# Kernel tuning notes

Hardware: AMD Instinct MI355X
Metric: run time of the kernel (lower is better)

The kernel has to match this reference:

```python
import jax, jax.numpy as jnp
import numpy as np

N_NODES = 32000
N_EDGES = 320000
N_GRAPHS = 1600
HID = 128
RBF = 32
ZDIM = 2 * HID + RBF  # CGConv concat dim = 288


def setup_inputs() -> dict:
    key = jax.random.key(0)
    ks = jax.random.split(key, 20)
    inp = {
        "x": jax.random.randint(ks[0], (N_NODES,), 0, 100),
        "edge_index": jax.random.randint(ks[1], (2, N_EDGES), 0, N_NODES),
        "edge_attr": jax.random.normal(ks[2], (N_EDGES, RBF), dtype=jnp.float32),
        "batch": jnp.sort(jax.random.randint(ks[3], (N_NODES,), 0, N_GRAPHS)),
        "emb": jax.random.normal(ks[4], (100, HID), dtype=jnp.float32) * 0.02,
    }
    s = 1.0 / np.sqrt(ZDIM)
    for i, k0 in zip((1, 2, 3), range(5, 11, 2)):
        inp[f"Wf{i}"] = jax.random.uniform(ks[k0], (ZDIM, HID), jnp.float32, -s, s)
        inp[f"bf{i}"] = jnp.zeros((HID,), jnp.float32)
        inp[f"Ws{i}"] = jax.random.uniform(ks[k0 + 1], (ZDIM, HID), jnp.float32, -s, s)
        inp[f"bs{i}"] = jnp.zeros((HID,), jnp.float32)
    sl = 1.0 / np.sqrt(HID)
    inp["Wlin"] = jax.random.uniform(ks[11], (HID, HID), jnp.float32, -sl, sl)
    inp["blin"] = jnp.zeros((HID,), jnp.float32)
    return inp


def _cgconv(h, src, dst, ea, Wf, bf, Ws, bs):
    # PyG CGConv: z = [x_i, x_j, e_ij]; msg = sigmoid(lin_f(z)) * softplus(lin_s(z)); out = x + sum_j msg
    z = jnp.concatenate([h[dst], h[src], ea], axis=1)  # [E, 288]
    msg = jax.nn.sigmoid(z @ Wf + bf) * jax.nn.softplus(z @ Ws + bs)  # [E, 128]
    return h + jax.ops.segment_sum(msg, dst, num_segments=N_NODES)


def reference(x, edge_index, edge_attr, batch, emb,
              Wf1, bf1, Ws1, bs1, Wf2, bf2, Ws2, bs2, Wf3, bf3, Ws3, bs3,
              Wlin, blin):
    src, dst = edge_index[0], edge_index[1]
    h = emb[x]  # [N, 128] embedding lookup
    h = jax.nn.relu(_cgconv(h, src, dst, edge_attr, Wf1, bf1, Ws1, bs1))
    h = jax.nn.relu(_cgconv(h, src, dst, edge_attr, Wf2, bf2, Ws2, bs2))
    h = jax.nn.relu(_cgconv(h, src, dst, edge_attr, Wf3, bf3, Ws3, bs3))
    # global mean pool over graphs
    sums = jax.ops.segment_sum(h, batch, num_segments=N_GRAPHS)  # [G, 128]
    cnt = jax.ops.segment_sum(jnp.ones((N_NODES,), h.dtype), batch, num_segments=N_GRAPHS)
    pooled = sums / jnp.maximum(cnt, 1.0)[:, None]
    return pooled @ Wlin + blin  # [G, 128]
```

## Files before the change

kernel.cpp:

```cpp
#include <hip/hip_runtime.h>
#include <math.h>

#define NN 32000
#define NE 320000
#define NG 1600
#define LOG2E 1.4426950408889634f
#define LN2   0.6931471805599453f

using frag_ab = __attribute__((ext_vector_type(8))) short;
using frag_cd = __attribute__((ext_vector_type(4))) float;
typedef float v2f __attribute__((ext_vector_type(2)));

static __device__ __forceinline__ unsigned short f2bf(float f) {
  unsigned u = __builtin_bit_cast(unsigned, f);
  unsigned r = u + 0x7fff + ((u >> 16) & 1);
  return (unsigned short)(r >> 16);
}
static __device__ __forceinline__ float bflo(unsigned u) {
  return __builtin_bit_cast(float, u << 16);
}
static __device__ __forceinline__ float bfhi(unsigned u) {
  return __builtin_bit_cast(float, u & 0xffff0000u);
}
static __device__ __forceinline__ float bfs(unsigned short u) {
  return __builtin_bit_cast(float, (unsigned)u << 16);
}
static __device__ __forceinline__ v2f unpk(unsigned u) {
  return (v2f){bflo(u), bfhi(u)};
}

__global__ __launch_bounds__(256) void k_misc(const int* __restrict__ x,
                                              const float* __restrict__ emb,
                                              const float* __restrict__ Wf1, const float* __restrict__ Ws1,
                                              const float* __restrict__ Wf2, const float* __restrict__ Ws2,
                                              const float* __restrict__ Wf3, const float* __restrict__ Ws3,
                                              unsigned short* __restrict__ hb,
                                              unsigned short* __restrict__ accumb,
                                              unsigned short* __restrict__ wedge,
                                              unsigned short* __restrict__ wgemm) {
  int b = blockIdx.x;
  int tid = threadIdx.x;
  if (b < 2000) {
    int idx = b * 256 + tid;
    int n = idx >> 4;
    int c8 = (idx & 15) << 3;
    const float* e = emb + (size_t)x[n] * 128 + c8;
    float4 v0 = *(const float4*)e;
    float4 v1 = *(const float4*)(e + 4);
    ushort4 p0, p1;
    p0.x = f2bf(v0.x); p0.y = f2bf(v0.y); p0.z = f2bf(v0.z); p0.w = f2bf(v0.w);
    p1.x = f2bf(v1.x); p1.y = f2bf(v1.y); p1.z = f2bf(v1.z); p1.w = f2bf(v1.w);
    unsigned short* hbp = hb + (size_t)n * 128 + c8;
    *(ushort4*)hbp = p0;
    *(ushort4*)(hbp + 4) = p1;
    *(uint4*)(accumb + (size_t)n * 128 + c8) = make_uint4(0, 0, 0, 0);
  } else if (b < 2096) {
    int idx = (b - 2000) * 256 + tid;
    int l = idx >> 13;
    int r = idx & 8191;
    int j = r & 7;
    int lane = (r >> 3) & 63;
    int wt = r >> 9;
    int w = wt >> 2, t = wt & 3;
    int c = lane & 15, q = lane >> 4;
    int k = q * 8 + j;
    const float* Wf = (l == 0) ? Wf1 : (l == 1) ? Wf2 : Wf3;
    const float* Ws = (l == 0) ? Ws1 : (l == 1) ? Ws2 : Ws3;
    const float* W = (t < 2) ? Wf : Ws;
    int ch = w * 32 + 2 * c + (t & 1);
    wedge[(size_t)l * 8192 + r] = f2bf(W[(size_t)(256 + k) * 128 + ch] * LOG2E);
  } else {
    int idx = (b - 2096) * 256 + tid;
    int l = idx >> 16;
    int r = idx & 65535;
    int cc = r >> 7;
    int k = r & 127;
    int p = (cc & ~31) + ((cc & 15) << 1) + ((cc >> 4) & 1);
    int ph = p & 255;
    int j = ph >> 2, sub = ph & 3;
    const float* Wf = (l == 0) ? Wf1 : (l == 1) ? Wf2 : Wf3;
    const float* Ws = (l == 0) ? Ws1 : (l == 1) ? Ws2 : Ws3;
    const float* W = (sub < 2) ? Wf : Ws;
    int ch = 2 * j + (sub & 1);
    int krow = ((p < 256) ? 0 : 128) + k;
    wgemm[(size_t)l * 65536 + cc * 128 + k] = f2bf(W[(size_t)krow * 128 + ch] * LOG2E);
  }
}

__global__ __launch_bounds__(256) void k_histb(const int* __restrict__ ei,
                                               const int* __restrict__ batch,
                                               int* __restrict__ counts,
                                               int* __restrict__ starts) {
  int b = blockIdx.x;
  int tid = threadIdx.x;
  if (b < 1250) {
    int e = b * 256 + tid;
    atomicAdd(counts + ei[NE + e], 1);
  } else {
    int n = (b - 1250) * 256 + tid;
    if (n > NN) return;
    if (n == NN) {
      starts[NG] = NN;
      int last = batch[NN - 1];
      for (int g = last + 1; g < NG; ++g) starts[g] = NN;
    } else if (n == 0) {
      int bb = batch[0];
      for (int g = 0; g <= bb; ++g) starts[g] = 0;
    } else {
      int b0 = batch[n - 1], b1 = batch[n];
      for (int g = b0 + 1; g <= b1; ++g) starts[g] = n;
    }
  }
}

__global__ __launch_bounds__(1024) void k_scan(const int* __restrict__ counts,
                                               int* __restrict__ offs) {
  __shared__ int part[1024];
  __shared__ int carry_s;
  int t = threadIdx.x;
  if (t == 0) carry_s = 0;
  __syncthreads();
  for (int chunk = 0; chunk < 4; ++chunk) {
    int base = chunk * 8192 + t * 8;
    int4 a = make_int4(0, 0, 0, 0), bq = make_int4(0, 0, 0, 0);
    bool full = (base + 8 <= NN);
    if (full) {
      a = *(const int4*)(counts + base);
      bq = *(const int4*)(counts + base + 4);
    }
    int e1 = a.x, e2 = e1 + a.y, e3 = e2 + a.z, e4 = e3 + a.w;
    int e5 = e4 + bq.x, e6 = e5 + bq.y, e7 = e6 + bq.z;
    int run = e7 + bq.w;
    part[t] = run;
    __syncthreads();
    for (int off = 1; off < 1024; off <<= 1) {
      int v = (t >= off) ? part[t - off] : 0;
      __syncthreads();
      part[t] += v;
      __syncthreads();
    }
    int excl = carry_s + ((t == 0) ? 0 : part[t - 1]);
    if (full) {
      int4 o0 = make_int4(excl, excl + e1, excl + e2, excl + e3);
      int4 o1 = make_int4(excl + e4, excl + e5, excl + e6, excl + e7);
      *(int4*)(offs + base) = o0;
      *(int4*)(offs + base + 4) = o1;
    }
    __syncthreads();
    if (t == 0) carry_s += part[1023];
    __syncthreads();
  }
}

__global__ __launch_bounds__(256) void k_scat1(const int* __restrict__ ei,
                                               int* __restrict__ offs,
                                               int* __restrict__ perm) {
  int e = blockIdx.x * 256 + threadIdx.x;
  int d = ei[NE + e];
  int pos = atomicAdd(offs + d, 1);
  perm[pos] = e;
}

__global__ __launch_bounds__(256) void k_s2g(const unsigned short* __restrict__ hb,
                                             const unsigned short* __restrict__ wgemmL,
                                             unsigned short* __restrict__ T,
                                             const int* __restrict__ ei,
                                             const float* __restrict__ ea,
                                             const int* __restrict__ perm,
                                             int* __restrict__ srcp,
                                             int* __restrict__ dstp,
                                             unsigned short* __restrict__ eab) {
  __shared__ short sA[64 * 136];
  __shared__ short sB[128 * 136];
  __shared__ int se[64];
  int b = blockIdx.x;
  int tid = threadIdx.x;
  if (b < 2000) {
    int m0 = (b >> 2) * 64;
    int n0 = (b & 3) * 128;
#pragma unroll
    for (int i = 0; i < 4; ++i) {
      int idx = tid + i * 256;
      int row = idx >> 4, chk = idx & 15;
      uint4 v = *(const uint4*)(hb + (size_t)(m0 + row) * 128 + chk * 8);
      *(uint4*)&sA[row * 136 + chk * 8] = v;
    }
#pragma unroll
    for (int i = 0; i < 8; ++i) {
      int idx = tid + i * 256;
      int col = idx >> 4, chk = idx & 15;
      uint4 v = *(const uint4*)(wgemmL + (size_t)(n0 + col) * 128 + chk * 8);
      *(uint4*)&sB[col * 136 + chk * 8] = v;
    }
    __syncthreads();
    int w = tid >> 6, lane = tid & 63, c = lane & 15, q = lane >> 4;
    frag_cd acc[4][2];
#pragma unroll
    for (int mt = 0; mt < 4; ++mt)
#pragma unroll
      for (int t = 0; t < 2; ++t) acc[mt][t] = (frag_cd){0.f, 0.f, 0.f, 0.f};
#pragma unroll
    for (int ks = 0; ks < 4; ++ks) {
      frag_ab Af[4], Bf[2];
#pragma unroll
      for (int mt = 0; mt < 4; ++mt)
        Af[mt] = *(const frag_ab*)&sA[(mt * 16 + c) * 136 + ks * 32 + q * 8];
#pragma unroll
      for (int t = 0; t < 2; ++t)
        Bf[t] = *(const frag_ab*)&sB[(w * 32 + t * 16 + c) * 136 + ks * 32 + q * 8];
#pragma unroll
      for (int mt = 0; mt < 4; ++mt)
#pragma unroll
        for (int t = 0; t < 2; ++t)
          acc[mt][t] = __builtin_amdgcn_mfma_f32_16x16x32_bf16(Af[mt], Bf[t], acc[mt][t], 0, 0, 0);
    }
    int nbase = n0 + w * 32 + 2 * c;
#pragma unroll
    for (int mt = 0; mt < 4; ++mt) {
#pragma unroll
      for (int r = 0; r < 4; ++r) {
        int node = m0 + mt * 16 + q * 4 + r;
        unsigned pk = (unsigned)f2bf(acc[mt][0][r]) | ((unsigned)f2bf(acc[mt][1][r]) << 16);
        *(unsigned*)(T + (size_t)node * 512 + nbase) = pk;
      }
    }
  } else {
    int base = (b - 2000) * 64;
    if (tid < 64) {
      int e = perm[base + tid];
      se[tid] = e;
      srcp[base + tid] = ei[e];
      dstp[base + tid] = ei[NE + e];
    }
    __syncthreads();
    int x = tid >> 2;
    int ck = tid & 3;
    int e = se[x];
    const float* a = ea + (size_t)e * 32 + ck * 8;
    float4 v0 = *(const float4*)a;
    float4 v1 = *(const float4*)(a + 4);
    int p = (((x >> 2) & 3) << 4) | ((x >> 4) << 2) | (x & 3);
    unsigned short* q = eab + (size_t)(base + p) * 32 + ck * 8;
    ushort4 o0, o1;
    o0.x = f2bf(v0.x); o0.y = f2bf(v0.y); o0.z = f2bf(v0.z); o0.w = f2bf(v0.w);
    o1.x = f2bf(v1.x); o1.y = f2bf(v1.y); o1.z = f2bf(v1.z); o1.w = f2bf(v1.w);
    *(ushort4*)q = o0;
    *(ushort4*)(q + 4) = o1;
  }
}

__global__ __launch_bounds__(256) void k_ugemm(unsigned short* __restrict__ hb,
                                               unsigned short* __restrict__ accumb,
                                               const unsigned short* __restrict__ wgemmL,
                                               unsigned short* __restrict__ T) {
  __shared__ short sA[64 * 136];
  __shared__ short sB[128 * 136];
  int m0 = blockIdx.x * 64;
  int tid = threadIdx.x;
#pragma unroll
  for (int i = 0; i < 4; ++i) {
    int idx = tid + i * 256;
    int row = idx >> 4, chk = idx & 15;
    size_t off = (size_t)(m0 + row) * 128 + chk * 8;
    uint4 a = *(uint4*)(accumb + off);
    uint4 hv = *(uint4*)(hb + off);
    float r0 = fmaxf(bflo(hv.x) + bflo(a.x), 0.f);
    float r1 = fmaxf(bfhi(hv.x) + bfhi(a.x), 0.f);
    float r2 = fmaxf(bflo(hv.y) + bflo(a.y), 0.f);
    float r3 = fmaxf(bfhi(hv.y) + bfhi(a.y), 0.f);
    float r4 = fmaxf(bflo(hv.z) + bflo(a.z), 0.f);
    float r5 = fmaxf(bfhi(hv.z) + bfhi(a.z), 0.f);
    float r6 = fmaxf(bflo(hv.w) + bflo(a.w), 0.f);
    float r7 = fmaxf(bfhi(hv.w) + bfhi(a.w), 0.f);
    uint4 o;
    o.x = (unsigned)f2bf(r0) | ((unsigned)f2bf(r1) << 16);
    o.y = (unsigned)f2bf(r2) | ((unsigned)f2bf(r3) << 16);
    o.z = (unsigned)f2bf(r4) | ((unsigned)f2bf(r5) << 16);
    o.w = (unsigned)f2bf(r6) | ((unsigned)f2bf(r7) << 16);
    *(uint4*)(hb + off) = o;
    *(uint4*)(accumb + off) = make_uint4(0, 0, 0, 0);
    *(uint4*)&sA[row * 136 + chk * 8] = o;
  }
  int w = tid >> 6, lane = tid & 63, c = lane & 15, q = lane >> 4;
#pragma unroll 1
  for (int nb = 0; nb < 4; ++nb) {
    int n0 = nb * 128;
    __syncthreads();
#pragma unroll
    for (int i = 0; i < 8; ++i) {
      int idx = tid + i * 256;
      int col = idx >> 4, chk = idx & 15;
      uint4 v = *(const uint4*)(wgemmL + (size_t)(n0 + col) * 128 + chk * 8);
      *(uint4*)&sB[col * 136 + chk * 8] = v;
    }
    __syncthreads();
    frag_cd acc[4][2];
#pragma unroll
    for (int mt = 0; mt < 4; ++mt)
#pragma unroll
      for (int t = 0; t < 2; ++t) acc[mt][t] = (frag_cd){0.f, 0.f, 0.f, 0.f};
#pragma unroll
    for (int ks = 0; ks < 4; ++ks) {
      frag_ab Af[4], Bf[2];
#pragma unroll
      for (int mt = 0; mt < 4; ++mt)
        Af[mt] = *(const frag_ab*)&sA[(mt * 16 + c) * 136 + ks * 32 + q * 8];
#pragma unroll
      for (int t = 0; t < 2; ++t)
        Bf[t] = *(const frag_ab*)&sB[(w * 32 + t * 16 + c) * 136 + ks * 32 + q * 8];
#pragma unroll
      for (int mt = 0; mt < 4; ++mt)
#pragma unroll
        for (int t = 0; t < 2; ++t)
          acc[mt][t] = __builtin_amdgcn_mfma_f32_16x16x32_bf16(Af[mt], Bf[t], acc[mt][t], 0, 0, 0);
    }
    int nbase = n0 + w * 32 + 2 * c;
#pragma unroll
    for (int mt = 0; mt < 4; ++mt) {
#pragma unroll
      for (int r = 0; r < 4; ++r) {
        int node = m0 + mt * 16 + q * 4 + r;
        unsigned pk = (unsigned)f2bf(acc[mt][0][r]) | ((unsigned)f2bf(acc[mt][1][r]) << 16);
        *(unsigned*)(T + (size_t)node * 512 + nbase) = pk;
      }
    }
  }
}

__global__ __launch_bounds__(512) void k_edge(const int* __restrict__ srcp,
                                              const int* __restrict__ dstp,
                                              const unsigned short* __restrict__ eab,
                                              const unsigned short* __restrict__ T,
                                              const unsigned short* __restrict__ wedgeL,
                                              const float* __restrict__ bf,
                                              const float* __restrict__ bs,
                                              unsigned short* __restrict__ accumb) {
  __shared__ short sA[128 * 40];
  __shared__ short sB[8192];
  __shared__ float sbf[128], sbs[128];
  __shared__ int sSrc[128], sDst[128];
  int tid = threadIdx.x;
  int e0 = blockIdx.x * 128;
  {
    int row = tid >> 2, qq = tid & 3;
    uint4 v = *(const uint4*)(eab + (size_t)e0 * 32 + tid * 8);
    *(uint4*)&sA[row * 40 + qq * 8] = v;
  }
#pragma unroll
  for (int i = 0; i < 2; ++i) {
    int idx = tid + i * 512;
    uint4 v = *(const uint4*)(wedgeL + idx * 8);
    *(uint4*)&sB[idx * 8] = v;
  }
  if (tid < 128) {
    sbf[tid] = bf[tid] * LOG2E;
    sbs[tid] = bs[tid] * LOG2E;
  } else if (tid < 256) {
    sSrc[tid - 128] = srcp[e0 + tid - 128] * 512 + 256;
  } else if (tid < 384) {
    sDst[tid - 256] = dstp[e0 + tid - 256] * 512;
  }
  __syncthreads();

  int wave = tid >> 6;
  int w = wave & 3;
  int eh = (wave >> 2) * 64;
  int lane = tid & 63;
  int c = lane & 15;
  int q = lane >> 4;

  int ch = w * 32 + 2 * c;
  int jo = ch * 2;
  v2f bfv = {sbf[ch], sbf[ch + 1]};
  v2f bsv = {sbs[ch], sbs[ch + 1]};

  frag_ab Af[4], Bf[4];
#pragma unroll
  for (int et = 0; et < 4; ++et)
    Af[et] = *(const frag_ab*)&sA[(eh + et * 16 + c) * 40 + q * 8];
#pragma unroll
  for (int t = 0; t < 4; ++t)
    Bf[t] = *(const frag_ab*)&sB[((w * 4 + t) * 64 + lane) * 8];

  frag_cd acc[4][4];
#pragma unroll
  for (int et = 0; et < 4; ++et) {
    acc[et][0] = (frag_cd){bfv.x, bfv.x, bfv.x, bfv.x};
    acc[et][1] = (frag_cd){bfv.y, bfv.y, bfv.y, bfv.y};
    acc[et][2] = (frag_cd){bsv.x, bsv.x, bsv.x, bsv.x};
    acc[et][3] = (frag_cd){bsv.y, bsv.y, bsv.y, bsv.y};
  }
#pragma unroll
  for (int et = 0; et < 4; ++et)
#pragma unroll
    for (int t = 0; t < 4; ++t)
      acc[et][t] = __builtin_amdgcn_mfma_f32_16x16x32_bf16(Af[et], Bf[t], acc[et][t], 0, 0, 0);

  int le0 = eh + q * 16;
  int prevd = sDst[le0];
  v2f av = {0.f, 0.f};

  uint2 dvb[2][4], svb[2][4];
#pragma unroll
  for (int i = 0; i < 4; ++i) {
    int e = le0 + i;
    dvb[0][i] = *(const uint2*)(T + sDst[e] + jo);
    svb[0][i] = *(const uint2*)(T + sSrc[e] + jo);
  }
#pragma unroll
  for (int g = 0; g < 4; ++g) {
    int cur = g & 1, nxt = cur ^ 1;
    if (g < 3) {
#pragma unroll
      for (int i = 0; i < 4; ++i) {
        int e = le0 + (g + 1) * 4 + i;
        dvb[nxt][i] = *(const uint2*)(T + sDst[e] + jo);
        svb[nxt][i] = *(const uint2*)(T + sSrc[e] + jo);
      }
    }
    v2f m[4];
#pragma unroll
    for (int i = 0; i < 4; ++i) {
      v2f xf = (v2f){acc[g][0][i], acc[g][1][i]} + unpk(dvb[cur][i].x) + unpk(svb[cur][i].x);
      v2f xs = (v2f){acc[g][2][i], acc[g][3][i]} + unpk(dvb[cur][i].y) + unpk(svb[cur][i].y);
      float g0 = __builtin_amdgcn_rcpf(1.f + __builtin_amdgcn_exp2f(-xf.x));
      float g1 = __builtin_amdgcn_rcpf(1.f + __builtin_amdgcn_exp2f(-xf.y));
      float sp0 = fmaxf(xs.x, 0.f) + __builtin_amdgcn_logf(1.f + __builtin_amdgcn_exp2f(-fabsf(xs.x)));
      float sp1 = fmaxf(xs.y, 0.f) + __builtin_amdgcn_logf(1.f + __builtin_amdgcn_exp2f(-fabsf(xs.y)));
      m[i] = (v2f){g0 * sp0, g1 * sp1};
    }
#pragma unroll
    for (int i = 0; i < 4; ++i) {
      int d = sDst[le0 + g * 4 + i];
      if (d != prevd) {
        v2f o = av * LN2;
        unsigned pk = (unsigned)f2bf(o.x) | ((unsigned)f2bf(o.y) << 16);
        unsigned short* p = accumb + (size_t)(prevd >> 2) + ch;
        asm volatile("global_atomic_pk_add_bf16 %0, %1, off" :: "v"(p), "v"(pk) : "memory");
        av = (v2f){0.f, 0.f};
        prevd = d;
      }
      av += m[i];
    }
  }
  {
    v2f o = av * LN2;
    unsigned pk = (unsigned)f2bf(o.x) | ((unsigned)f2bf(o.y) << 16);
    unsigned short* p = accumb + (size_t)(prevd >> 2) + ch;
    asm volatile("global_atomic_pk_add_bf16 %0, %1, off" :: "v"(p), "v"(pk) : "memory");
  }
}

__global__ __launch_bounds__(128) void k_pool_final(const unsigned short* __restrict__ hb,
                                                    const unsigned short* __restrict__ accumb,
                                                    const int* __restrict__ starts,
                                                    const float* __restrict__ Wlin,
                                                    const float* __restrict__ blin,
                                                    float* __restrict__ out) {
  __shared__ float p[128];
  int g = blockIdx.x, c = threadIdx.x;
  int s0 = starts[g], s1 = starts[g + 1];
  float acc = 0.f;
  for (int n = s0; n < s1; ++n) {
    float hv = bfs(hb[(size_t)n * 128 + c]);
    float av = bfs(accumb[(size_t)n * 128 + c]);
    acc += fmaxf(hv + av, 0.f);
  }
  float inv = 1.f / fmaxf((float)(s1 - s0), 1.f);
  p[c] = acc * inv;
  __syncthreads();
  float o = blin[c];
#pragma unroll 8
  for (int k = 0; k < 128; ++k) o += p[k] * Wlin[k * 128 + c];
  out[(size_t)g * 128 + c] = o;
}

extern "C" void kernel_launch(void* const* d_in, const int* in_sizes, int n_in,
                              void* d_out, int out_size, void* d_ws, size_t ws_size,
                              hipStream_t stream) {
  const int* x = (const int*)d_in[0];
  const int* ei = (const int*)d_in[1];
  const float* ea = (const float*)d_in[2];
  const int* batch = (const int*)d_in[3];
  const float* emb = (const float*)d_in[4];
  const float* Wf[3] = {(const float*)d_in[5], (const float*)d_in[9], (const float*)d_in[13]};
  const float* bf[3] = {(const float*)d_in[6], (const float*)d_in[10], (const float*)d_in[14]};
  const float* Wsm[3] = {(const float*)d_in[7], (const float*)d_in[11], (const float*)d_in[15]};
  const float* bs[3] = {(const float*)d_in[8], (const float*)d_in[12], (const float*)d_in[16]};
  const float* Wlin = (const float*)d_in[17];
  const float* blin = (const float*)d_in[18];
  float* out = (float*)d_out;

  char* ws = (char*)d_ws;
  unsigned short* hb = (unsigned short*)ws;     ws += (size_t)NN * 128 * 2;
  unsigned short* accumb = (unsigned short*)ws; ws += (size_t)NN * 128 * 2;
  unsigned short* T = (unsigned short*)ws;      ws += (size_t)NN * 512 * 2;
  unsigned short* eab = (unsigned short*)ws;    ws += (size_t)NE * 32 * 2;
  unsigned short* wedge = (unsigned short*)ws;  ws += 3 * 8192 * 2;
  unsigned short* wgemm = (unsigned short*)ws;  ws += 3 * 65536 * 2;
  int* counts = (int*)ws;                       ws += (size_t)NN * 4;
  int* offs = (int*)ws;                         ws += (size_t)NN * 4;
  int* srcp = (int*)ws;                         ws += (size_t)NE * 4;
  int* dstp = (int*)ws;                         ws += (size_t)NE * 4;
  int* perm = (int*)ws;                         ws += (size_t)NE * 4;
  int* starts = (int*)ws;                       ws += (size_t)(NG + 1) * 4;

  hipMemsetAsync(counts, 0, (size_t)NN * 4, stream);
  k_misc<<<2864, 256, 0, stream>>>(x, emb, Wf[0], Wsm[0], Wf[1], Wsm[1], Wf[2], Wsm[2],
                                   hb, accumb, wedge, wgemm);
  k_histb<<<1376, 256, 0, stream>>>(ei, batch, counts, starts);
  k_scan<<<1, 1024, 0, stream>>>(counts, offs);
  k_scat1<<<1250, 256, 0, stream>>>(ei, offs, perm);
  k_s2g<<<7000, 256, 0, stream>>>(hb, wgemm, T, ei, ea, perm, srcp, dstp, eab);
  for (int l = 0; l < 3; ++l) {
    if (l > 0)
      k_ugemm<<<500, 256, 0, stream>>>(hb, accumb, wgemm + (size_t)l * 65536, T);
    k_edge<<<2500, 512, 0, stream>>>(srcp, dstp, eab, T, wedge + (size_t)l * 8192,
                                     bf[l], bs[l], accumb);
  }
  k_pool_final<<<1600, 128, 0, stream>>>(hb, accumb, starts, Wlin, blin, out);
}
```

Before: 346.3 us.

## Merge weight prep with histogram and fuse embedding lookup into first GEMM

Combines the weight-conversion kernel and the edge-histogram/graph-start kernel into one launch. The embedding lookup, bf16 conversion and accumulator zeroing move into the layer-1 node GEMM. Each GEMM block now builds its 64-row A tile directly from the embedding and loops over all four 128-column B tiles, instead of four blocks each reloading A from global memory. This removes one launch and a round trip of the node features through memory, at the cost of fewer, longer GEMM blocks (500 instead of 2000) with a serial loop over N tiles.

```diff
diff --git a/kernel.cpp b/kernel.cpp
--- a/kernel.cpp
+++ b/kernel.cpp
@@ -29,33 +29,19 @@
   return (v2f){bflo(u), bfhi(u)};
 }
 
-__global__ __launch_bounds__(256) void k_misc(const int* __restrict__ x,
-                                              const float* __restrict__ emb,
-                                              const float* __restrict__ Wf1, const float* __restrict__ Ws1,
-                                              const float* __restrict__ Wf2, const float* __restrict__ Ws2,
-                                              const float* __restrict__ Wf3, const float* __restrict__ Ws3,
-                                              unsigned short* __restrict__ hb,
-                                              unsigned short* __restrict__ accumb,
-                                              unsigned short* __restrict__ wedge,
-                                              unsigned short* __restrict__ wgemm) {
+__global__ __launch_bounds__(256) void k_prephist(const float* __restrict__ Wf1, const float* __restrict__ Ws1,
+                                                  const float* __restrict__ Wf2, const float* __restrict__ Ws2,
+                                                  const float* __restrict__ Wf3, const float* __restrict__ Ws3,
+                                                  const int* __restrict__ ei,
+                                                  const int* __restrict__ batch,
+                                                  unsigned short* __restrict__ wedge,
+                                                  unsigned short* __restrict__ wgemm,
+                                                  int* __restrict__ counts,
+                                                  int* __restrict__ starts) {
   int b = blockIdx.x;
   int tid = threadIdx.x;
-  if (b < 2000) {
+  if (b < 96) {
     int idx = b * 256 + tid;
-    int n = idx >> 4;
-    int c8 = (idx & 15) << 3;
-    const float* e = emb + (size_t)x[n] * 128 + c8;
-    float4 v0 = *(const float4*)e;
-    float4 v1 = *(const float4*)(e + 4);
-    ushort4 p0, p1;
-    p0.x = f2bf(v0.x); p0.y = f2bf(v0.y); p0.z = f2bf(v0.z); p0.w = f2bf(v0.w);
-    p1.x = f2bf(v1.x); p1.y = f2bf(v1.y); p1.z = f2bf(v1.z); p1.w = f2bf(v1.w);
-    unsigned short* hbp = hb + (size_t)n * 128 + c8;
-    *(ushort4*)hbp = p0;
-    *(ushort4*)(hbp + 4) = p1;
-    *(uint4*)(accumb + (size_t)n * 128 + c8) = make_uint4(0, 0, 0, 0);
-  } else if (b < 2096) {
-    int idx = (b - 2000) * 256 + tid;
     int l = idx >> 13;
     int r = idx & 8191;
     int j = r & 7;
@@ -69,8 +55,8 @@
     const float* W = (t < 2) ? Wf : Ws;
     int ch = w * 32 + 2 * c + (t & 1);
     wedge[(size_t)l * 8192 + r] = f2bf(W[(size_t)(256 + k) * 128 + ch] * LOG2E);
-  } else {
-    int idx = (b - 2096) * 256 + tid;
+  } else if (b < 864) {
+    int idx = (b - 96) * 256 + tid;
     int l = idx >> 16;
     int r = idx & 65535;
     int cc = r >> 7;
@@ -84,20 +70,11 @@
     int ch = 2 * j + (sub & 1);
     int krow = ((p < 256) ? 0 : 128) + k;
     wgemm[(size_t)l * 65536 + cc * 128 + k] = f2bf(W[(size_t)krow * 128 + ch] * LOG2E);
-  }
-}
-
-__global__ __launch_bounds__(256) void k_histb(const int* __restrict__ ei,
-                                               const int* __restrict__ batch,
-                                               int* __restrict__ counts,
-                                               int* __restrict__ starts) {
-  int b = blockIdx.x;
-  int tid = threadIdx.x;
-  if (b < 1250) {
-    int e = b * 256 + tid;
+  } else if (b < 2114) {
+    int e = (b - 864) * 256 + tid;
     atomicAdd(counts + ei[NE + e], 1);
   } else {
-    int n = (b - 1250) * 256 + tid;
+    int n = (b - 2114) * 256 + tid;
     if (n > NN) return;
     if (n == NN) {
       starts[NG] = NN;
@@ -161,9 +138,12 @@
   perm[pos] = e;
 }
 
-__global__ __launch_bounds__(256) void k_s2g(const unsigned short* __restrict__ hb,
+__global__ __launch_bounds__(256) void k_s2g(const int* __restrict__ x,
+                                             const float* __restrict__ emb,
                                              const unsigned short* __restrict__ wgemmL,
                                              unsigned short* __restrict__ T,
+                                             unsigned short* __restrict__ hb,
+                                             unsigned short* __restrict__ accumb,
                                              const int* __restrict__ ei,
                                              const float* __restrict__ ea,
                                              const int* __restrict__ perm,
@@ -175,57 +155,72 @@
   __shared__ int se[64];
   int b = blockIdx.x;
   int tid = threadIdx.x;
-  if (b < 2000) {
-    int m0 = (b >> 2) * 64;
-    int n0 = (b & 3) * 128;
+  if (b < 500) {
+    int m0 = b * 64;
 #pragma unroll
     for (int i = 0; i < 4; ++i) {
       int idx = tid + i * 256;
-      int row = idx >> 4, chk = idx & 15;
-      uint4 v = *(const uint4*)(hb + (size_t)(m0 + row) * 128 + chk * 8);
-      *(uint4*)&sA[row * 136 + chk * 8] = v;
-    }
-#pragma unroll
-    for (int i = 0; i < 8; ++i) {
-      int idx = tid + i * 256;
-      int col = idx >> 4, chk = idx & 15;
-      uint4 v = *(const uint4*)(wgemmL + (size_t)(n0 + col) * 128 + chk * 8);
-      *(uint4*)&sB[col * 136 + chk * 8] = v;
-    }
-    __syncthreads();
+      int row = idx >> 4, c8 = (idx & 15) << 3;
+      int n = m0 + row;
+      const float* e = emb + (size_t)x[n] * 128 + c8;
+      float4 v0 = *(const float4*)e;
+      float4 v1 = *(const float4*)(e + 4);
+      uint4 o;
+      o.x = (unsigned)f2bf(v0.x) | ((unsigned)f2bf(v0.y) << 16);
+      o.y = (unsigned)f2bf(v0.z) | ((unsigned)f2bf(v0.w) << 16);
+      o.z = (unsigned)f2bf(v1.x) | ((unsigned)f2bf(v1.y) << 16);
+      o.w = (unsigned)f2bf(v1.z) | ((unsigned)f2bf(v1.w) << 16);
+      size_t off = (size_t)n * 128 + c8;
+      *(uint4*)(hb + off) = o;
+      *(uint4*)(accumb + off) = make_uint4(0, 0, 0, 0);
+      *(uint4*)&sA[row * 136 + c8] = o;
+    }
     int w = tid >> 6, lane = tid & 63, c = lane & 15, q = lane >> 4;
-    frag_cd acc[4][2];
-#pragma unroll
-    for (int mt = 0; mt < 4; ++mt)
-#pragma unroll
-      for (int t = 0; t < 2; ++t) acc[mt][t] = (frag_cd){0.f, 0.f, 0.f, 0.f};
-#pragma unroll
-    for (int ks = 0; ks < 4; ++ks) {
-      frag_ab Af[4], Bf[2];
+#pragma unroll 1
+    for (int nb = 0; nb < 4; ++nb) {
+      int n0 = nb * 128;
+      __syncthreads();
+#pragma unroll
+      for (int i = 0; i < 8; ++i) {
+        int idx = tid + i * 256;
+        int col = idx >> 4, chk = idx & 15;
+        uint4 v = *(const uint4*)(wgemmL + (size_t)(n0 + col) * 128 + chk * 8);
+        *(uint4*)&sB[col * 136 + chk * 8] = v;
+      }
+      __syncthreads();
+      frag_cd acc[4][2];
 #pragma unroll
       for (int mt = 0; mt < 4; ++mt)
-        Af[mt] = *(const frag_ab*)&sA[(mt * 16 + c) * 136 + ks * 32 + q * 8];
-#pragma unroll
-      for (int t = 0; t < 2; ++t)
-        Bf[t] = *(const frag_ab*)&sB[(w * 32 + t * 16 + c) * 136 + ks * 32 + q * 8];
-#pragma unroll
-      for (int mt = 0; mt < 4; ++mt)
+#pragma unroll
+        for (int t = 0; t < 2; ++t) acc[mt][t] = (frag_cd){0.f, 0.f, 0.f, 0.f};
+#pragma unroll
+      for (int ks = 0; ks < 4; ++ks) {
+        frag_ab Af[4], Bf[2];
+#pragma unroll
+        for (int mt = 0; mt < 4; ++mt)
+          Af[mt] = *(const frag_ab*)&sA[(mt * 16 + c) * 136 + ks * 32 + q * 8];
 #pragma unroll
         for (int t = 0; t < 2; ++t)
-          acc[mt][t] = __builtin_amdgcn_mfma_f32_16x16x32_bf16(Af[mt], Bf[t], acc[mt][t], 0, 0, 0);
-    }
-    int nbase = n0 + w * 32 + 2 * c;
-#pragma unroll
-    for (int mt = 0; mt < 4; ++mt) {
-#pragma unroll
-      for (int r = 0; r < 4; ++r) {
-        int node = m0 + mt * 16 + q * 4 + r;
-        unsigned pk = (unsigned)f2bf(acc[mt][0][r]) | ((unsigned)f2bf(acc[mt][1][r]) << 16);
-        *(unsigned*)(T + (size_t)node * 512 + nbase) = pk;
+          Bf[t] = *(const frag_ab*)&sB[(w * 32 + t * 16 + c) * 136 + ks * 32 + q * 8];
+#pragma unroll
+        for (int mt = 0; mt < 4; ++mt)
+#pragma unroll
+          for (int t = 0; t < 2; ++t)
+            acc[mt][t] = __builtin_amdgcn_mfma_f32_16x16x32_bf16(Af[mt], Bf[t], acc[mt][t], 0, 0, 0);
       }
+      int nbase = n0 + w * 32 + 2 * c;
+#pragma unroll
+      for (int mt = 0; mt < 4; ++mt) {
+#pragma unroll
+        for (int r = 0; r < 4; ++r) {
+          int node = m0 + mt * 16 + q * 4 + r;
+          unsigned pk = (unsigned)f2bf(acc[mt][0][r]) | ((unsigned)f2bf(acc[mt][1][r]) << 16);
+          *(unsigned*)(T + (size_t)node * 512 + nbase) = pk;
+        }
+      }
     }
   } else {
-    int base = (b - 2000) * 64;
+    int base = (b - 500) * 64;
     if (tid < 64) {
       int e = perm[base + tid];
       se[tid] = e;
@@ -233,13 +228,13 @@
       dstp[base + tid] = ei[NE + e];
     }
     __syncthreads();
-    int x = tid >> 2;
+    int xs = tid >> 2;
     int ck = tid & 3;
-    int e = se[x];
+    int e = se[xs];
     const float* a = ea + (size_t)e * 32 + ck * 8;
     float4 v0 = *(const float4*)a;
     float4 v1 = *(const float4*)(a + 4);
-    int p = (((x >> 2) & 3) << 4) | ((x >> 4) << 2) | (x & 3);
+    int p = (((xs >> 2) & 3) << 4) | ((xs >> 4) << 2) | (xs & 3);
     unsigned short* q = eab + (size_t)(base + p) * 32 + ck * 8;
     ushort4 o0, o1;
     o0.x = f2bf(v0.x); o0.y = f2bf(v0.y); o0.z = f2bf(v0.z); o0.w = f2bf(v0.w);
@@ -506,12 +501,12 @@
   int* starts = (int*)ws;                       ws += (size_t)(NG + 1) * 4;
 
   hipMemsetAsync(counts, 0, (size_t)NN * 4, stream);
-  k_misc<<<2864, 256, 0, stream>>>(x, emb, Wf[0], Wsm[0], Wf[1], Wsm[1], Wf[2], Wsm[2],
-                                   hb, accumb, wedge, wgemm);
-  k_histb<<<1376, 256, 0, stream>>>(ei, batch, counts, starts);
+  k_prephist<<<2240, 256, 0, stream>>>(Wf[0], Wsm[0], Wf[1], Wsm[1], Wf[2], Wsm[2],
+                                       ei, batch, wedge, wgemm, counts, starts);
   k_scan<<<1, 1024, 0, stream>>>(counts, offs);
   k_scat1<<<1250, 256, 0, stream>>>(ei, offs, perm);
-  k_s2g<<<7000, 256, 0, stream>>>(hb, wgemm, T, ei, ea, perm, srcp, dstp, eab);
+  k_s2g<<<5500, 256, 0, stream>>>(x, emb, wgemm, T, hb, accumb, ei, ea, perm,
+                                  srcp, dstp, eab);
   for (int l = 0; l < 3; ++l) {
     if (l > 0)
       k_ugemm<<<500, 256, 0, stream>>>(hb, accumb, wgemm + (size_t)l * 65536, T);
```

Measured after the change: 344.0 us. No clear change (-0.6%).
